# Kernel tuning notes

Hardware: AMD Instinct MI355X
Metric: run time of the kernel (lower is better)

Reference implementation:

```python
import jax, jax.numpy as jnp
import numpy as np

B, TMAX, N = 8192, 2048, 2  # batch, max sequence length, hidden states


def setup_inputs() -> dict:
    key = jax.random.key(0)
    k1, k2 = jax.random.split(key)
    x = jax.random.randint(k1, (B, TMAX), 0, 2, dtype=jnp.int32)          # binary observations
    T = jax.random.randint(k2, (B, 1), 1, TMAX + 1, dtype=jnp.int32)     # valid lengths in [1, TMAX]
    combined_input = jnp.concatenate([x, T], axis=1)                      # (B, TMAX+1)
    # learned parameters (initial values hardcoded in the torch module)
    state_prior_logits = jnp.array([0.3, 0.7], dtype=jnp.float32)
    transition_logits = jnp.array([[0.9, 0.1], [0.85, 0.15]], dtype=jnp.float32)
    emission_logits = jnp.array([[0.8, 0.2], [0.6, 0.4]], dtype=jnp.float32)
    return {
        "combined_input": combined_input,
        "state_prior_logits": state_prior_logits,
        "transition_logits": transition_logits,
        "emission_logits": emission_logits,
    }


def reference(combined_input, state_prior_logits, transition_logits, emission_logits):
    x = combined_input[:, :-1]          # (B, TMAX) int observations
    T = combined_input[:, -1]           # (B,) lengths
    priors = jax.nn.softmax(state_prior_logits)                 # (N,)
    A = jax.nn.softmax(transition_logits, axis=1)               # (N, N)
    emT = jax.nn.softmax(emission_logits, axis=1).T             # (M, N): emT[obs] == emission_probs[:, obs]

    alpha0 = emT[x[:, 0]] * priors                              # (B, N)

    def step(alpha, xt):
        # alpha_t[:, n] = p(obs_t | n) * sum_m alpha_{t-1}[:, m] * A[m, n]
        alpha = emT[xt] * (alpha @ A)
        return alpha, alpha.sum(axis=-1)

    _, sums = jax.lax.scan(step, alpha0, x[:, 1:].T)            # sums: (TMAX-1, B)
    probs = jnp.concatenate([alpha0.sum(axis=-1)[None, :], sums], axis=0).T  # (B, TMAX)
    final_probs = jnp.take_along_axis(probs, (T - 1)[:, None], axis=1)       # (B, 1)
    return final_probs
```

## Files before the change

kernel.cpp:

```cpp
#include <hip/hip_runtime.h>

#define TMAX_C 2048
#define ROWLEN (TMAX_C + 1)

__global__ __launch_bounds__(256, 8) void hmm_fwd_kernel(
    const int* __restrict__ combined,
    const float* __restrict__ sp,
    const float* __restrict__ tr,
    const float* __restrict__ emi,
    float* __restrict__ out, int B)
{
    const int lane = threadIdx.x & 63;
    const int b = blockIdx.x * (blockDim.x >> 6) + (threadIdx.x >> 6);
    if (b >= B) return;

    const int* __restrict__ row = combined + (size_t)b * ROWLEN;
    const int T = row[TMAX_C];
    const int steps = T - 1;
    const int nwords = (steps + 63) >> 6;

    int a[32];
    #pragma unroll
    for (int g = 0; g < 4; ++g) {
        if ((g << 3) < nwords) {
            #pragma unroll
            for (int u = 0; u < 8; ++u) {
                a[(g << 3) + u] = row[1 + ((((g << 3) + u)) << 6) + lane];
            }
        }
    }

    float p0 = __expf(sp[0]), p1 = __expf(sp[1]);
    { float s = p0 + p1; p0 /= s; p1 /= s; }
    float A00, A01, A10, A11;
    { float e0 = __expf(tr[0]), e1 = __expf(tr[1]); float s = e0 + e1; A00 = e0/s; A01 = e1/s; }
    { float e0 = __expf(tr[2]), e1 = __expf(tr[3]); float s = e0 + e1; A10 = e0/s; A11 = e1/s; }
    float em00, em01, em10, em11;
    { float e0 = __expf(emi[0]), e1 = __expf(emi[1]); float s = e0 + e1; em00 = e0/s; em01 = e1/s; }
    { float e0 = __expf(emi[2]), e1 = __expf(emi[3]); float s = e0 + e1; em10 = e0/s; em11 = e1/s; }

    const float M0_00 = A00*em00, M0_01 = A01*em10, M0_10 = A10*em00, M0_11 = A11*em10;
    const float M1_00 = A00*em01, M1_01 = A01*em11, M1_10 = A10*em01, M1_11 = A11*em11;

    const int my_word = lane >> 1;
    unsigned long long my_mask = 0ULL;
    #pragma unroll
    for (int g = 0; g < 4; ++g) {
        if ((g << 3) < nwords) {
            #pragma unroll
            for (int u = 0; u < 8; ++u) {
                const int w = (g << 3) + u;
                const unsigned long long m = __ballot(a[w] != 0);
                if (w == my_word) my_mask = m;
            }
        }
    }
    const unsigned int bits = (lane & 1) ? (unsigned int)(my_mask >> 32)
                                         : (unsigned int)my_mask;
    const int cnt = min(max(steps - (lane << 5), 0), 32);

    float P00 = 1.f, P01 = 0.f, P10 = 0.f, P11 = 1.f;
    #pragma unroll
    for (int j = 0; j < 32; ++j) {
        const bool bit = (bits >> j) & 1u;
        const float m00 = bit ? M1_00 : M0_00;
        const float m01 = bit ? M1_01 : M0_01;
        const float m10 = bit ? M1_10 : M0_10;
        const float m11 = bit ? M1_11 : M0_11;
        const float n00 = P00*m00 + P01*m10;
        const float n01 = P00*m01 + P01*m11;
        const float n10 = P10*m00 + P11*m10;
        const float n11 = P10*m01 + P11*m11;
        const bool ok = j < cnt;
        P00 = ok ? n00 : P00;
        P01 = ok ? n01 : P01;
        P10 = ok ? n10 : P10;
        P11 = ok ? n11 : P11;
    }

    #pragma unroll
    for (int off = 1; off < 64; off <<= 1) {
        const float q00 = __shfl_down(P00, off);
        const float q01 = __shfl_down(P01, off);
        const float q10 = __shfl_down(P10, off);
        const float q11 = __shfl_down(P11, off);
        if (lane + off < 64) {
            const float n00 = P00*q00 + P01*q10;
            const float n01 = P00*q01 + P01*q11;
            const float n10 = P10*q00 + P11*q10;
            const float n11 = P10*q01 + P11*q11;
            P00 = n00; P01 = n01; P10 = n10; P11 = n11;
        }
    }

    if (lane == 0) {
        const int x0 = row[0];
        const float a0 = (x0 ? em01 : em00) * p0;
        const float a1 = (x0 ? em11 : em10) * p1;
        const float v0 = a0*P00 + a1*P10;
        const float v1 = a0*P01 + a1*P11;
        out[b] = v0 + v1;
    }
}

extern "C" void kernel_launch(void* const* d_in, const int* in_sizes, int n_in,
                              void* d_out, int out_size, void* d_ws, size_t ws_size,
                              hipStream_t stream) {
    const int*   combined = (const int*)d_in[0];
    const float* sp       = (const float*)d_in[1];
    const float* tr       = (const float*)d_in[2];
    const float* emi      = (const float*)d_in[3];
    float* out = (float*)d_out;

    const int B = out_size;
    const int waves_per_block = 4;
    const int grid = (B + waves_per_block - 1) / waves_per_block;
    hmm_fwd_kernel<<<grid, 256, 0, stream>>>(combined, sp, tr, emi, out, B);
}
```

Measured before the change: 103.5 us.

## Pipeline observation loads with ballots and adapt per-lane step count to sequence length

Loads observation words in two 8-word double-buffered groups interleaved with ballot packing, which cuts the live register array from 32 to 16 entries. Work is now split evenly across lanes by the actual word count W instead of a fixed 32 bits per lane, so each lane runs a loop of length W rather than 32. Bits are fetched with cross-lane shuffles that may straddle two words. The row index is made wave-uniform with readfirstlane, x0 is loaded early, and the branch on lane bounds is dropped from the shuffle reduction. The runtime-bound loop may add loop overhead.

```diff
diff --git a/kernel.cpp b/kernel.cpp
--- a/kernel.cpp
+++ b/kernel.cpp
@@ -14,21 +14,42 @@
     const int b = blockIdx.x * (blockDim.x >> 6) + (threadIdx.x >> 6);
     if (b >= B) return;
 
-    const int* __restrict__ row = combined + (size_t)b * ROWLEN;
-    const int T = row[TMAX_C];
+    const int ub = __builtin_amdgcn_readfirstlane(b);
+    const int* __restrict__ row = combined + (size_t)ub * ROWLEN;
+    const int T  = row[TMAX_C];
+    const int x0 = row[0];
     const int steps = T - 1;
-    const int nwords = (steps + 63) >> 6;
+    const int W = (steps + 63) >> 6;
 
-    int a[32];
-    #pragma unroll
-    for (int g = 0; g < 4; ++g) {
-        if ((g << 3) < nwords) {
-            #pragma unroll
-            for (int u = 0; u < 8; ++u) {
-                a[(g << 3) + u] = row[1 + ((((g << 3) + u)) << 6) + lane];
-            }
-        }
-    }
+    unsigned wlo = 0u, whi = 0u;
+    int A0[8], A1[8];
+
+#define LOADG(g, buf)                                                   \
+    do {                                                                \
+        _Pragma("unroll")                                               \
+        for (int u = 0; u < 8; ++u) {                                   \
+            const int w = ((g) << 3) + u;                               \
+            if (w < W) (buf)[u] = row[1 + (w << 6) + lane];             \
+        }                                                               \
+    } while (0)
+
+#define BALLOTG(g, buf)                                                 \
+    do {                                                                \
+        _Pragma("unroll")                                               \
+        for (int u = 0; u < 8; ++u) {                                   \
+            const int w = ((g) << 3) + u;                               \
+            if (w < W) {                                                \
+                const unsigned long long m = __ballot((buf)[u] != 0);   \
+                if (lane == w) {                                        \
+                    wlo = (unsigned)m;                                  \
+                    whi = (unsigned)(m >> 32);                          \
+                }                                                       \
+            }                                                           \
+        }                                                               \
+    } while (0)
+
+    LOADG(0, A0);
+    LOADG(1, A1);
 
     float p0 = __expf(sp[0]), p1 = __expf(sp[1]);
     { float s = p0 + p1; p0 /= s; p1 /= s; }
@@ -42,26 +63,33 @@
     const float M0_00 = A00*em00, M0_01 = A01*em10, M0_10 = A10*em00, M0_11 = A11*em10;
     const float M1_00 = A00*em01, M1_01 = A01*em11, M1_10 = A10*em01, M1_11 = A11*em11;
 
-    const int my_word = lane >> 1;
-    unsigned long long my_mask = 0ULL;
-    #pragma unroll
-    for (int g = 0; g < 4; ++g) {
-        if ((g << 3) < nwords) {
-            #pragma unroll
-            for (int u = 0; u < 8; ++u) {
-                const int w = (g << 3) + u;
-                const unsigned long long m = __ballot(a[w] != 0);
-                if (w == my_word) my_mask = m;
-            }
-        }
-    }
-    const unsigned int bits = (lane & 1) ? (unsigned int)(my_mask >> 32)
-                                         : (unsigned int)my_mask;
-    const int cnt = min(max(steps - (lane << 5), 0), 32);
+    BALLOTG(0, A0);
+    LOADG(2, A0);
+    BALLOTG(1, A1);
+    LOADG(3, A1);
+    BALLOTG(2, A0);
+    BALLOTG(3, A1);
+#undef LOADG
+#undef BALLOTG
+
+    const int idx = lane * W;
+    const int w0  = idx >> 6;
+    const int off = idx & 63;
+    const unsigned u0lo = (unsigned)__shfl((int)wlo, w0);
+    const unsigned u0hi = (unsigned)__shfl((int)whi, w0);
+    const unsigned u1lo = (unsigned)__shfl((int)wlo, w0 + 1);
+    const unsigned long long v64 = ((unsigned long long)u0hi << 32) | u0lo;
+    unsigned bits = (unsigned)(v64 >> off);
+    if (off + W > 64)
+        bits |= (u1lo << (64 - off));
+
+    int cnt = steps - idx;
+    cnt = cnt < 0 ? 0 : cnt;
+    cnt = cnt > W ? W : cnt;
 
     float P00 = 1.f, P01 = 0.f, P10 = 0.f, P11 = 1.f;
-    #pragma unroll
-    for (int j = 0; j < 32; ++j) {
+    #pragma unroll 4
+    for (int j = 0; j < W; ++j) {
         const bool bit = (bits >> j) & 1u;
         const float m00 = bit ? M1_00 : M0_00;
         const float m01 = bit ? M1_01 : M0_01;
@@ -79,22 +107,19 @@
     }
 
     #pragma unroll
-    for (int off = 1; off < 64; off <<= 1) {
-        const float q00 = __shfl_down(P00, off);
-        const float q01 = __shfl_down(P01, off);
-        const float q10 = __shfl_down(P10, off);
-        const float q11 = __shfl_down(P11, off);
-        if (lane + off < 64) {
-            const float n00 = P00*q00 + P01*q10;
-            const float n01 = P00*q01 + P01*q11;
-            const float n10 = P10*q00 + P11*q10;
-            const float n11 = P10*q01 + P11*q11;
-            P00 = n00; P01 = n01; P10 = n10; P11 = n11;
-        }
+    for (int off2 = 1; off2 < 64; off2 <<= 1) {
+        const float q00 = __shfl_down(P00, off2);
+        const float q01 = __shfl_down(P01, off2);
+        const float q10 = __shfl_down(P10, off2);
+        const float q11 = __shfl_down(P11, off2);
+        const float n00 = P00*q00 + P01*q10;
+        const float n01 = P00*q01 + P01*q11;
+        const float n10 = P10*q00 + P11*q10;
+        const float n11 = P10*q01 + P11*q11;
+        P00 = n00; P01 = n01; P10 = n10; P11 = n11;
     }
 
     if (lane == 0) {
-        const int x0 = row[0];
         const float a0 = (x0 ? em01 : em00) * p0;
         const float a1 = (x0 ? em11 : em10) * p1;
         const float v0 = a0*P00 + a1*P10;
```

After: 101.8 us. No clear change (-1.6%).
